# Kernel optimization log

Measured on AMD Instinct MI355X. Metric: run time of the kernel, lower is better.

Reference implementation:

```python
import jax, jax.numpy as jnp
import numpy as np
from functools import partial

EPS = 1e-6

def rmsnorm(x, w):
    rms = jnp.sqrt(jnp.mean(x * x, axis=-1, keepdims=True) + EPS)
    return x * w / rms

def causal_dwconv(x, w):
    # x: [B, T, D], w: [D, 1, k] depthwise kernel (torch Conv1d layout)
    D = x.shape[-1]
    k = w.shape[-1]
    xt = jnp.transpose(x, (0, 2, 1))  # [B, D, T]
    out = jax.lax.conv_general_dilated(
        xt, w, window_strides=(1,), padding=[(k - 1, 0)],
        dimension_numbers=("NCH", "OIH", "NCH"), feature_group_count=D)
    return jnp.transpose(out, (0, 2, 1))  # [B, T, D]

def setup_inputs() -> dict:
    key = jax.random.key(0)
    B, T, D, F, S = 2, 4096, 1024, 4096, 4096
    ks = jax.random.split(key, 20)
    s = 0.02
    return {
        "x": jax.random.normal(ks[0], (B, T, D), jnp.float32),
        "h_prev": jnp.zeros((B, D), jnp.float32),
        "norm1_w": jnp.ones((D,), jnp.float32),
        "conv3_w": jax.random.normal(ks[1], (D, 1, 3), jnp.float32) * s,
        "conv7_w": jax.random.normal(ks[2], (D, 1, 7), jnp.float32) * s,
        "conv15_w": jax.random.normal(ks[3], (D, 1, 15), jnp.float32) * s,
        "mix_w": jax.random.normal(ks[4], (D, D), jnp.float32) * s,
        "norm2_w": jnp.ones((D,), jnp.float32),
        "Wz_w": jax.random.normal(ks[5], (D, D), jnp.float32) * s,
        "Wz_b": jnp.zeros((D,), jnp.float32),
        "Wh_w": jax.random.normal(ks[6], (D, D), jnp.float32) * s,
        "Wh_b": jnp.zeros((D,), jnp.float32),
        "norm3_w": jnp.ones((D,), jnp.float32),
        "slot_keys": jax.random.normal(ks[7], (S, D), jnp.float32) * s,
        "slot_values": jax.random.normal(ks[8], (S, D), jnp.float32) * s,
        "projq_w": jax.random.normal(ks[9], (D, D), jnp.float32) * s,
        "projout_w": jax.random.normal(ks[10], (D, D), jnp.float32) * s,
        "norm4_w": jnp.ones((D,), jnp.float32),
        "gate_w": jax.random.normal(ks[11], (F, D), jnp.float32) * s,
        "up_w": jax.random.normal(ks[12], (F, D), jnp.float32) * s,
        "down_w": jax.random.normal(ks[13], (D, F), jnp.float32) * s,
    }

def resonance_forward(x, h_prev, norm1_w, conv3_w, conv7_w, conv15_w, mix_w,
                      norm2_w, Wz_w, Wz_b, Wh_w, Wh_b, norm3_w, slot_keys,
                      slot_values, projq_w, projout_w, norm4_w, gate_w, up_w, down_w):
    B, T, D = x.shape
    top_k = 2
    # 1. multi-scale causal conv block
    xn = rmsnorm(x, norm1_w)
    conv = causal_dwconv(xn, conv3_w) + causal_dwconv(xn, conv7_w) + causal_dwconv(xn, conv15_w)
    x = x + conv @ mix_w.T
    # 2. MinGRU: precompute gates, then linear recurrence via scan
    xn = rmsnorm(x, norm2_w)
    z = jax.nn.sigmoid(xn @ Wz_w.T + Wz_b)        # [B, T, D]
    h_tilde = xn @ Wh_w.T + Wh_b                  # [B, T, D]
    def step(h, zh):
        zt, ht = zh
        h = (1.0 - zt) * h + zt * ht
        return h, h
    h_last, hs = jax.lax.scan(step, h_prev,
                              (jnp.swapaxes(z, 0, 1), jnp.swapaxes(h_tilde, 0, 1)))
    x = x + jnp.swapaxes(hs, 0, 1)
    # 3. slot memory with top-k routing
    xn = rmsnorm(x, norm3_w)
    q = xn @ projq_w.T
    scores = (q @ slot_keys.T) / jnp.sqrt(jnp.asarray(D, x.dtype))  # [B, T, S]
    topk_vals, topk_ids = jax.lax.top_k(scores, top_k)              # [B, T, k]
    attn = jax.nn.softmax(topk_vals, axis=-1)
    gathered = slot_values[topk_ids]                                # [B, T, k, D]
    retrieved = jnp.einsum("btk,btkd->btd", attn, gathered)
    x = x + retrieved @ projout_w.T
    # 4. SwiGLU FFN
    xn = rmsnorm(x, norm4_w)
    ff = (jax.nn.silu(xn @ gate_w.T) * (xn @ up_w.T)) @ down_w.T
    x = x + ff
    return x, h_last

def reference(x, h_prev, norm1_w, conv3_w, conv7_w, conv15_w, mix_w, norm2_w,
              Wz_w, Wz_b, Wh_w, Wh_b, norm3_w, slot_keys, slot_values,
              projq_w, projout_w, norm4_w, gate_w, up_w, down_w):
    return resonance_forward(x, h_prev, norm1_w, conv3_w, conv7_w, conv15_w,
                             mix_w, norm2_w, Wz_w, Wz_b, Wh_w, Wh_b, norm3_w,
                             slot_keys, slot_values, projq_w, projout_w,
                             norm4_w, gate_w, up_w, down_w)
```

## Files before the change

kernel.cpp:

```cpp
#include <hip/hip_runtime.h>
#include <hip/hip_bf16.h>
#include <cstdint>

#define BB   2
#define TT   4096
#define DD   1024
#define FF   4096
#define SS   4096
#define MTOK (BB * TT)
#define NCHUNK 32
#define TCHUNK 128

typedef __bf16 bf16x8 __attribute__((ext_vector_type(8)));
typedef float  f32x4  __attribute__((ext_vector_type(4)));
typedef __attribute__((address_space(3))) char lds_char;
typedef __attribute__((address_space(1))) char g_char;

__global__ __launch_bounds__(256) void cvt_kernel(const float* __restrict__ s,
                                                  __hip_bfloat16* __restrict__ d,
                                                  int n4) {
  int i = blockIdx.x * 256 + threadIdx.x;
  if (i < n4) {
    float4 v = ((const float4*)s)[i];
    union { ushort4 u; __hip_bfloat16 h[4]; } p;
    p.h[0] = __float2bfloat16(v.x);
    p.h[1] = __float2bfloat16(v.y);
    p.h[2] = __float2bfloat16(v.z);
    p.h[3] = __float2bfloat16(v.w);
    ((ushort4*)d)[i] = p.u;
  }
}

__global__ void wcomb_kernel(const float* __restrict__ w3, const float* __restrict__ w7,
                             const float* __restrict__ w15, float* __restrict__ wc) {
  int d = blockIdx.x * 256 + threadIdx.x;
  if (d >= DD) return;
  for (int j = 0; j < 16; j++) {
    float v = 0.f;
    if (j < 15) {
      v = w15[d * 15 + (14 - j)];
      if (j < 7) v += w7[d * 7 + (6 - j)];
      if (j < 3) v += w3[d * 3 + (2 - j)];
    }
    wc[d * 16 + j] = v;
  }
}

template <int OUT_BF16>
__global__ __launch_bounds__(256) void rms_kernel(const float* __restrict__ x,
                                                  const float* __restrict__ w,
                                                  float* __restrict__ of,
                                                  __hip_bfloat16* __restrict__ ob) {
  const int row = blockIdx.x;
  const int tid = threadIdx.x;
  float4 v = ((const float4*)(x + (size_t)row * DD))[tid];
  float ss = v.x * v.x + v.y * v.y + v.z * v.z + v.w * v.w;
  for (int off = 32; off > 0; off >>= 1) ss += __shfl_down(ss, off, 64);
  __shared__ float wsum[4];
  if ((tid & 63) == 0) wsum[tid >> 6] = ss;
  __syncthreads();
  float tot = wsum[0] + wsum[1] + wsum[2] + wsum[3];
  float rinv = 1.0f / sqrtf(tot * (1.0f / DD) + 1e-6f);
  float4 wg = ((const float4*)w)[tid];
  float4 o;
  o.x = v.x * wg.x * rinv; o.y = v.y * wg.y * rinv;
  o.z = v.z * wg.z * rinv; o.w = v.w * wg.w * rinv;
  if (OUT_BF16) {
    union { ushort4 u; __hip_bfloat16 h[4]; } p;
    p.h[0] = __float2bfloat16(o.x); p.h[1] = __float2bfloat16(o.y);
    p.h[2] = __float2bfloat16(o.z); p.h[3] = __float2bfloat16(o.w);
    ((ushort4*)ob)[(size_t)row * 256 + tid] = p.u;
  } else {
    ((float4*)of)[(size_t)row * 256 + tid] = o;
  }
}

__global__ __launch_bounds__(256) void conv_kernel(const float* __restrict__ xn,
                                                   const float* __restrict__ wc,
                                                   __hip_bfloat16* __restrict__ outp) {
  __shared__ float xt[78][64];
  __shared__ float wt[64][15];
  const int b = blockIdx.z, t0 = blockIdx.x * 64, d0 = blockIdx.y * 64;
  const int tid = threadIdx.x;
  const int dl = tid & 63;
  for (int idx = tid; idx < 64 * 15; idx += 256) {
    int d = idx / 15, j = idx % 15;
    wt[d][j] = wc[(d0 + d) * 16 + j];
  }
  for (int r = tid >> 6; r < 78; r += 4) {
    int t = t0 - 14 + r;
    xt[r][dl] = (t >= 0) ? xn[((size_t)b * TT + t) * DD + d0 + dl] : 0.f;
  }
  __syncthreads();
  for (int tl = tid >> 6; tl < 64; tl += 4) {
    float acc = 0.f;
#pragma unroll
    for (int j = 0; j < 15; j++) acc += wt[dl][j] * xt[tl + 14 - j][dl];
    outp[((size_t)b * TT + t0 + tl) * DD + d0 + dl] = __float2bfloat16(acc);
  }
}

template <int EPI>
__global__ __launch_bounds__(256, 2) void gemm_bt(
    const __hip_bfloat16* __restrict__ A, const __hip_bfloat16* __restrict__ Bm,
    const int M, const int N, const int K,
    const float* __restrict__ resid, float* __restrict__ outf,
    __hip_bfloat16* __restrict__ outb,
    const float* __restrict__ bias0, const float* __restrict__ bias1,
    const __hip_bfloat16* __restrict__ mulin) {
  __shared__ __align__(16) __hip_bfloat16 As[128 * 32];
  __shared__ __align__(16) __hip_bfloat16 Bs[128 * 32];
  const int tid = threadIdx.x;
  const int lane = tid & 63;
  const int wave = tid >> 6;
  const int fm = lane & 15, fq = lane >> 4;
  const int tileN = blockIdx.x * 128;
  const int tileM = blockIdx.y * 128;
  const int wm = (wave & 1) * 64, wn = (wave >> 1) * 64;

  f32x4 acc[4][4] = {};

  const int srow = tid >> 2;
  const int scol = (tid & 3) * 8;
  const __hip_bfloat16* gA = A + (size_t)(tileM + srow) * K + scol;
  const __hip_bfloat16* gB = Bm + (size_t)(tileN + srow) * K + scol;
  lds_char* ldsA = (lds_char*)(&As[0]);
  lds_char* ldsB = (lds_char*)(&Bs[0]);
  const int wbyte = wave * 1024;

  for (int k0 = 0; k0 < K; k0 += 32) {
    __syncthreads();
    __builtin_amdgcn_global_load_lds((g_char*)(void*)(gA + k0),                  ldsA + wbyte,        16, 0, 0);
    __builtin_amdgcn_global_load_lds((g_char*)(void*)(gA + k0 + (size_t)64 * K), ldsA + wbyte + 4096, 16, 0, 0);
    __builtin_amdgcn_global_load_lds((g_char*)(void*)(gB + k0),                  ldsB + wbyte,        16, 0, 0);
    __builtin_amdgcn_global_load_lds((g_char*)(void*)(gB + k0 + (size_t)64 * K), ldsB + wbyte + 4096, 16, 0, 0);
    __syncthreads();
    bf16x8 af[4], bfr[4];
#pragma unroll
    for (int i = 0; i < 4; i++) {
      af[i]  = *(const bf16x8*)(As + (wm + i * 16 + fm) * 32 + fq * 8);
      bfr[i] = *(const bf16x8*)(Bs + (wn + i * 16 + fm) * 32 + fq * 8);
    }
#pragma unroll
    for (int i = 0; i < 4; i++)
#pragma unroll
      for (int j = 0; j < 4; j++)
        acc[i][j] = __builtin_amdgcn_mfma_f32_16x16x32_bf16(af[i], bfr[j], acc[i][j], 0, 0, 0);
  }

#pragma unroll
  for (int i = 0; i < 4; i++) {
#pragma unroll
    for (int j = 0; j < 4; j++) {
      const int c = tileN + wn + j * 16 + fm;
#pragma unroll
      for (int r = 0; r < 4; r++) {
        const int rw = tileM + wm + i * 16 + fq * 4 + r;
        const size_t idx = (size_t)rw * N + c;
        float v = acc[i][j][r];
        if constexpr (EPI == 0) {
          outf[idx] = resid[idx] + v;
        } else if constexpr (EPI == 1) {
          v += (c < DD) ? bias0[c] : bias1[c - DD];
          if (c < DD) v = 1.f / (1.f + __expf(-v));
          outf[idx] = v;
        } else if constexpr (EPI == 2) {
          outb[idx] = __float2bfloat16(v);
        } else if constexpr (EPI == 3) {
          outf[idx] = v;
        } else if constexpr (EPI == 4) {
          outb[idx] = __float2bfloat16(v / (1.f + __expf(-v)));
        } else {
          outb[idx] = __float2bfloat16(v * __bfloat162float(mulin[idx]));
        }
      }
    }
  }
}

__global__ __launch_bounds__(256) void scan_pass1(const float* __restrict__ zht,
                                                  float* __restrict__ cA,
                                                  float* __restrict__ cB) {
  const int b = blockIdx.z, c = blockIdx.y;
  const int d = blockIdx.x * 256 + threadIdx.x;
  const float* base = zht + (size_t)b * TT * 2048;
  float A = 1.f, Bc = 0.f;
  const int t0 = c * TCHUNK;
  for (int t = t0; t < t0 + TCHUNK; t++) {
    const float* rowp = base + (size_t)t * 2048;
    float z = rowp[d];
    float h = rowp[DD + d];
    float om = 1.f - z;
    A *= om;
    Bc = om * Bc + z * h;
  }
  size_t idx = ((size_t)b * NCHUNK + c) * DD + d;
  cA[idx] = A;
  cB[idx] = Bc;
}

__global__ __launch_bounds__(256) void scan_pass2(const float* __restrict__ hp,
                                                  const float* __restrict__ cA,
                                                  const float* __restrict__ cB,
                                                  float* __restrict__ hstart,
                                                  float* __restrict__ hlast) {
  const int b = blockIdx.y;
  const int d = blockIdx.x * 256 + threadIdx.x;
  float h = hp[b * DD + d];
  for (int c = 0; c < NCHUNK; c++) {
    size_t idx = ((size_t)b * NCHUNK + c) * DD + d;
    hstart[idx] = h;
    h = cA[idx] * h + cB[idx];
  }
  hlast[b * DD + d] = h;
}

__global__ __launch_bounds__(256) void scan_pass3(const float* __restrict__ zht,
                                                  const float* __restrict__ hstart,
                                                  float* __restrict__ x) {
  const int b = blockIdx.z, c = blockIdx.y;
  const int d = blockIdx.x * 256 + threadIdx.x;
  const float* base = zht + (size_t)b * TT * 2048;
  float h = hstart[((size_t)b * NCHUNK + c) * DD + d];
  const int t0 = c * TCHUNK;
  for (int t = t0; t < t0 + TCHUNK; t++) {
    const float* rowp = base + (size_t)t * 2048;
    float z = rowp[d];
    float ht = rowp[DD + d];
    h = (1.f - z) * h + z * ht;
    x[((size_t)b * TT + t) * DD + d] += h;
  }
}

__global__ __launch_bounds__(256) void topk_kernel(const float* __restrict__ scores,
                                                   const float* __restrict__ sv,
                                                   __hip_bfloat16* __restrict__ ret) {
  const int row = blockIdx.x;
  const int tid = threadIdx.x;
  const float* sr = scores + (size_t)row * SS;
  float v0 = -3.4e38f, v1 = -3.4e38f;
  int i0 = 0x7fffffff, i1 = 0x7fffffff;
  for (int j = tid; j < SS; j += 256) {
    float v = sr[j];
    if (v > v0) { v1 = v0; i1 = i0; v0 = v; i0 = j; }
    else if (v > v1) { v1 = v; i1 = j; }
  }
#define TKMERGE(w0, j0, w1, j1)                                              \
  {                                                                          \
    if (w0 > v0 || (w0 == v0 && j0 < i0)) {                                  \
      float t0v = v0; int t0i = i0; v0 = w0; i0 = j0;                        \
      if (t0v > w1 || (t0v == w1 && t0i < j1)) { v1 = t0v; i1 = t0i; }       \
      else { v1 = w1; i1 = j1; }                                             \
    } else {                                                                 \
      if (w0 > v1 || (w0 == v1 && j0 < i1)) { v1 = w0; i1 = j0; }            \
    }                                                                        \
  }
  for (int off = 32; off > 0; off >>= 1) {
    float w0 = __shfl_down(v0, off, 64), w1 = __shfl_down(v1, off, 64);
    int   j0 = __shfl_down(i0, off, 64), j1 = __shfl_down(i1, off, 64);
    TKMERGE(w0, j0, w1, j1);
  }
  __shared__ float wv0[4], wv1[4];
  __shared__ int   wi0[4], wi1[4];
  __shared__ float sattn[2];
  __shared__ int   sidx[2];
  if ((tid & 63) == 0) { int w = tid >> 6; wv0[w] = v0; wv1[w] = v1; wi0[w] = i0; wi1[w] = i1; }
  __syncthreads();
  if (tid == 0) {
    v0 = wv0[0]; i0 = wi0[0]; v1 = wv1[0]; i1 = wi1[0];
    for (int w = 1; w < 4; w++) { TKMERGE(wv0[w], wi0[w], wv1[w], wi1[w]); }
    float s0 = v0 * (1.f / 32.f), s1 = v1 * (1.f / 32.f);
    float e = __expf(s1 - s0);
    float denom = 1.f + e;
    sattn[0] = 1.f / denom;
    sattn[1] = e / denom;
    sidx[0] = i0; sidx[1] = i1;
  }
  __syncthreads();
  float a0 = sattn[0], a1 = sattn[1];
  const float4* r0 = (const float4*)(sv + (size_t)sidx[0] * DD);
  const float4* r1 = (const float4*)(sv + (size_t)sidx[1] * DD);
  float4 u = r0[tid], w4 = r1[tid];
  union { ushort4 u; __hip_bfloat16 h[4]; } p;
  p.h[0] = __float2bfloat16(a0 * u.x + a1 * w4.x);
  p.h[1] = __float2bfloat16(a0 * u.y + a1 * w4.y);
  p.h[2] = __float2bfloat16(a0 * u.z + a1 * w4.z);
  p.h[3] = __float2bfloat16(a0 * u.w + a1 * w4.w);
  ((ushort4*)(ret + (size_t)row * DD))[tid] = p.u;
#undef TKMERGE
}

extern "C" void kernel_launch(void* const* d_in, const int* in_sizes, int n_in,
                              void* d_out, int out_size, void* d_ws, size_t ws_size,
                              hipStream_t stream) {
  (void)in_sizes; (void)n_in; (void)out_size; (void)ws_size;
  const float* x_in   = (const float*)d_in[0];
  const float* h_prev = (const float*)d_in[1];
  const float* n1w    = (const float*)d_in[2];
  const float* w3     = (const float*)d_in[3];
  const float* w7     = (const float*)d_in[4];
  const float* w15    = (const float*)d_in[5];
  const float* mixw   = (const float*)d_in[6];
  const float* n2w    = (const float*)d_in[7];
  const float* wzw    = (const float*)d_in[8];
  const float* wzb    = (const float*)d_in[9];
  const float* whw    = (const float*)d_in[10];
  const float* whb    = (const float*)d_in[11];
  const float* n3w    = (const float*)d_in[12];
  const float* slotk  = (const float*)d_in[13];
  const float* slotv  = (const float*)d_in[14];
  const float* pqw    = (const float*)d_in[15];
  const float* pow_   = (const float*)d_in[16];
  const float* n4w    = (const float*)d_in[17];
  const float* gatew  = (const float*)d_in[18];
  const float* upw    = (const float*)d_in[19];
  const float* downw  = (const float*)d_in[20];
  float* out = (float*)d_out;

  char* ws = (char*)d_ws;
  size_t o = 0;
  auto alloc = [&](size_t bytes) {
    size_t r = o;
    o += (bytes + 255) & ~(size_t)255;
    return r;
  };
  __hip_bfloat16* wmix = (__hip_bfloat16*)(ws + alloc((size_t)DD * DD * 2));
  __hip_bfloat16* wzht = (__hip_bfloat16*)(ws + alloc((size_t)2 * DD * DD * 2));
  __hip_bfloat16* wpq  = (__hip_bfloat16*)(ws + alloc((size_t)DD * DD * 2));
  __hip_bfloat16* wsk  = (__hip_bfloat16*)(ws + alloc((size_t)SS * DD * 2));
  __hip_bfloat16* wpo  = (__hip_bfloat16*)(ws + alloc((size_t)DD * DD * 2));
  __hip_bfloat16* wg   = (__hip_bfloat16*)(ws + alloc((size_t)FF * DD * 2));
  __hip_bfloat16* wu   = (__hip_bfloat16*)(ws + alloc((size_t)FF * DD * 2));
  __hip_bfloat16* wd   = (__hip_bfloat16*)(ws + alloc((size_t)DD * FF * 2));
  float* wcomb = (float*)(ws + alloc((size_t)DD * 16 * 4));
  float* xws   = (float*)(ws + alloc((size_t)MTOK * DD * 4));
  __hip_bfloat16* xnb  = (__hip_bfloat16*)(ws + alloc((size_t)MTOK * DD * 2));
  __hip_bfloat16* qb   = (__hip_bfloat16*)(ws + alloc((size_t)MTOK * DD * 2));
  __hip_bfloat16* retr = (__hip_bfloat16*)(ws + alloc((size_t)MTOK * DD * 2));
  float* scanA  = (float*)(ws + alloc((size_t)BB * NCHUNK * DD * 4));
  float* scanB  = (float*)(ws + alloc((size_t)BB * NCHUNK * DD * 4));
  float* hstart = (float*)(ws + alloc((size_t)BB * NCHUNK * DD * 4));
  char* big = ws + alloc((size_t)MTOK * FF * 4);
  float* xn1f           = (float*)big;
  __hip_bfloat16* convb = (__hip_bfloat16*)(big + (size_t)MTOK * DD * 4);
  float* zht            = (float*)big;
  float* scores         = (float*)big;
  __hip_bfloat16* sg    = (__hip_bfloat16*)big;
  __hip_bfloat16* ffin  = (__hip_bfloat16*)(big + (size_t)MTOK * FF * 2);

  auto cvt = [&](const float* s, __hip_bfloat16* dp, int n) {
    cvt_kernel<<<n / 1024, 256, 0, stream>>>(s, dp, n / 4);
  };
  cvt(mixw, wmix, DD * DD);
  cvt(wzw, wzht, DD * DD);
  cvt(whw, wzht + (size_t)DD * DD, DD * DD);
  cvt(pqw, wpq, DD * DD);
  cvt(slotk, wsk, SS * DD);
  cvt(pow_, wpo, DD * DD);
  cvt(gatew, wg, FF * DD);
  cvt(upw, wu, FF * DD);
  cvt(downw, wd, DD * FF);
  wcomb_kernel<<<DD / 256, 256, 0, stream>>>(w3, w7, w15, wcomb);

  rms_kernel<0><<<MTOK, 256, 0, stream>>>(x_in, n1w, xn1f, nullptr);
  conv_kernel<<<dim3(TT / 64, DD / 64, BB), 256, 0, stream>>>(xn1f, wcomb, convb);
  gemm_bt<0><<<dim3(DD / 128, MTOK / 128), 256, 0, stream>>>(
      convb, wmix, MTOK, DD, DD, x_in, xws, nullptr, nullptr, nullptr, nullptr);

  rms_kernel<1><<<MTOK, 256, 0, stream>>>(xws, n2w, nullptr, xnb);
  gemm_bt<1><<<dim3(2048 / 128, MTOK / 128), 256, 0, stream>>>(
      xnb, wzht, MTOK, 2048, DD, nullptr, zht, nullptr, wzb, whb, nullptr);
  scan_pass1<<<dim3(DD / 256, NCHUNK, BB), 256, 0, stream>>>(zht, scanA, scanB);
  scan_pass2<<<dim3(DD / 256, BB), 256, 0, stream>>>(h_prev, scanA, scanB, hstart,
                                                     out + (size_t)MTOK * DD);
  scan_pass3<<<dim3(DD / 256, NCHUNK, BB), 256, 0, stream>>>(zht, hstart, xws);

  rms_kernel<1><<<MTOK, 256, 0, stream>>>(xws, n3w, nullptr, xnb);
  gemm_bt<2><<<dim3(DD / 128, MTOK / 128), 256, 0, stream>>>(
      xnb, wpq, MTOK, DD, DD, nullptr, nullptr, qb, nullptr, nullptr, nullptr);
  gemm_bt<3><<<dim3(SS / 128, MTOK / 128), 256, 0, stream>>>(
      qb, wsk, MTOK, SS, DD, nullptr, scores, nullptr, nullptr, nullptr, nullptr);
  topk_kernel<<<MTOK, 256, 0, stream>>>(scores, slotv, retr);
  gemm_bt<0><<<dim3(DD / 128, MTOK / 128), 256, 0, stream>>>(
      retr, wpo, MTOK, DD, DD, xws, xws, nullptr, nullptr, nullptr, nullptr);

  rms_kernel<1><<<MTOK, 256, 0, stream>>>(xws, n4w, nullptr, xnb);
  gemm_bt<4><<<dim3(FF / 128, MTOK / 128), 256, 0, stream>>>(
      xnb, wg, MTOK, FF, DD, nullptr, nullptr, sg, nullptr, nullptr, nullptr);
  gemm_bt<5><<<dim3(FF / 128, MTOK / 128), 256, 0, stream>>>(
      xnb, wu, MTOK, FF, DD, nullptr, nullptr, ffin, nullptr, nullptr, sg);
  gemm_bt<0><<<dim3(DD / 128, MTOK / 128), 256, 0, stream>>>(
      ffin, wd, MTOK, DD, FF, xws, out, nullptr, nullptr, nullptr, nullptr);
}
```

Measured before the change: 908.7 us.

## Store intermediates in bf16, fuse weight conversions, and remap GEMM tiles per XCD

Several intermediates (the norm1 output, the gate/candidate activations, and the routing scores) are now stored in bf16 instead of fp32. This roughly halves the memory traffic for the conv, scan and top-k kernels, and top-k now reads its scores with 8-wide vector loads. The nine weight conversion launches are merged into a single kernel that finds its segment through an offset table. GEMM blocks are remapped so that each XCD works on a contiguous band of M-tiles, aiming for better L2 reuse. Storing scores in bf16 risks changing top-k selection when scores are close or tied, and z/h lose precision before the scan.

```diff
diff --git a/kernel.cpp b/kernel.cpp
--- a/kernel.cpp
+++ b/kernel.cpp
@@ -16,19 +16,25 @@
 typedef __attribute__((address_space(3))) char lds_char;
 typedef __attribute__((address_space(1))) char g_char;
 
-__global__ __launch_bounds__(256) void cvt_kernel(const float* __restrict__ s,
-                                                  __hip_bfloat16* __restrict__ d,
-                                                  int n4) {
-  int i = blockIdx.x * 256 + threadIdx.x;
-  if (i < n4) {
-    float4 v = ((const float4*)s)[i];
-    union { ushort4 u; __hip_bfloat16 h[4]; } p;
-    p.h[0] = __float2bfloat16(v.x);
-    p.h[1] = __float2bfloat16(v.y);
-    p.h[2] = __float2bfloat16(v.z);
-    p.h[3] = __float2bfloat16(v.w);
-    ((ushort4*)d)[i] = p.u;
-  }
+struct CvtArgs {
+  const float* src[9];
+  __hip_bfloat16* dst[9];
+  int off4[10];
+};
+
+__global__ __launch_bounds__(256) void cvt_all_kernel(CvtArgs a) {
+  int g = blockIdx.x * 256 + threadIdx.x;
+  if (g >= a.off4[9]) return;
+  int s = 0;
+  while (g >= a.off4[s + 1]) s++;
+  int i = g - a.off4[s];
+  float4 v = ((const float4*)a.src[s])[i];
+  union { ushort4 u; __hip_bfloat16 h[4]; } p;
+  p.h[0] = __float2bfloat16(v.x);
+  p.h[1] = __float2bfloat16(v.y);
+  p.h[2] = __float2bfloat16(v.z);
+  p.h[3] = __float2bfloat16(v.w);
+  ((ushort4*)a.dst[s])[i] = p.u;
 }
 
 __global__ void wcomb_kernel(const float* __restrict__ w3, const float* __restrict__ w7,
@@ -46,10 +52,8 @@
   }
 }
 
-template <int OUT_BF16>
 __global__ __launch_bounds__(256) void rms_kernel(const float* __restrict__ x,
                                                   const float* __restrict__ w,
-                                                  float* __restrict__ of,
                                                   __hip_bfloat16* __restrict__ ob) {
   const int row = blockIdx.x;
   const int tid = threadIdx.x;
@@ -62,20 +66,15 @@
   float tot = wsum[0] + wsum[1] + wsum[2] + wsum[3];
   float rinv = 1.0f / sqrtf(tot * (1.0f / DD) + 1e-6f);
   float4 wg = ((const float4*)w)[tid];
-  float4 o;
-  o.x = v.x * wg.x * rinv; o.y = v.y * wg.y * rinv;
-  o.z = v.z * wg.z * rinv; o.w = v.w * wg.w * rinv;
-  if (OUT_BF16) {
-    union { ushort4 u; __hip_bfloat16 h[4]; } p;
-    p.h[0] = __float2bfloat16(o.x); p.h[1] = __float2bfloat16(o.y);
-    p.h[2] = __float2bfloat16(o.z); p.h[3] = __float2bfloat16(o.w);
-    ((ushort4*)ob)[(size_t)row * 256 + tid] = p.u;
-  } else {
-    ((float4*)of)[(size_t)row * 256 + tid] = o;
-  }
-}
-
-__global__ __launch_bounds__(256) void conv_kernel(const float* __restrict__ xn,
+  union { ushort4 u; __hip_bfloat16 h[4]; } p;
+  p.h[0] = __float2bfloat16(v.x * wg.x * rinv);
+  p.h[1] = __float2bfloat16(v.y * wg.y * rinv);
+  p.h[2] = __float2bfloat16(v.z * wg.z * rinv);
+  p.h[3] = __float2bfloat16(v.w * wg.w * rinv);
+  ((ushort4*)ob)[(size_t)row * 256 + tid] = p.u;
+}
+
+__global__ __launch_bounds__(256) void conv_kernel(const __hip_bfloat16* __restrict__ xn,
                                                    const float* __restrict__ wc,
                                                    __hip_bfloat16* __restrict__ outp) {
   __shared__ float xt[78][64];
@@ -89,7 +88,7 @@
   }
   for (int r = tid >> 6; r < 78; r += 4) {
     int t = t0 - 14 + r;
-    xt[r][dl] = (t >= 0) ? xn[((size_t)b * TT + t) * DD + d0 + dl] : 0.f;
+    xt[r][dl] = (t >= 0) ? __bfloat162float(xn[((size_t)b * TT + t) * DD + d0 + dl]) : 0.f;
   }
   __syncthreads();
   for (int tl = tid >> 6; tl < 64; tl += 4) {
@@ -114,8 +113,15 @@
   const int lane = tid & 63;
   const int wave = tid >> 6;
   const int fm = lane & 15, fq = lane >> 4;
-  const int tileN = blockIdx.x * 128;
-  const int tileM = blockIdx.y * 128;
+
+  const int nT = gridDim.x;
+  const int lin = blockIdx.y * nT + blockIdx.x;
+  const int xcd = lin & 7;
+  const int idx_ = lin >> 3;
+  const int mq = idx_ / nT;
+  const int tileM = (xcd * (gridDim.y >> 3) + mq) * 128;
+  const int tileN = (idx_ - mq * nT) * 128;
+
   const int wm = (wave & 1) * 64, wn = (wave >> 1) * 64;
 
   f32x4 acc[4][4] = {};
@@ -163,11 +169,9 @@
         } else if constexpr (EPI == 1) {
           v += (c < DD) ? bias0[c] : bias1[c - DD];
           if (c < DD) v = 1.f / (1.f + __expf(-v));
-          outf[idx] = v;
+          outb[idx] = __float2bfloat16(v);
         } else if constexpr (EPI == 2) {
           outb[idx] = __float2bfloat16(v);
-        } else if constexpr (EPI == 3) {
-          outf[idx] = v;
         } else if constexpr (EPI == 4) {
           outb[idx] = __float2bfloat16(v / (1.f + __expf(-v)));
         } else {
@@ -178,18 +182,18 @@
   }
 }
 
-__global__ __launch_bounds__(256) void scan_pass1(const float* __restrict__ zht,
+__global__ __launch_bounds__(256) void scan_pass1(const __hip_bfloat16* __restrict__ zht,
                                                   float* __restrict__ cA,
                                                   float* __restrict__ cB) {
   const int b = blockIdx.z, c = blockIdx.y;
   const int d = blockIdx.x * 256 + threadIdx.x;
-  const float* base = zht + (size_t)b * TT * 2048;
+  const __hip_bfloat16* base = zht + (size_t)b * TT * 2048;
   float A = 1.f, Bc = 0.f;
   const int t0 = c * TCHUNK;
   for (int t = t0; t < t0 + TCHUNK; t++) {
-    const float* rowp = base + (size_t)t * 2048;
-    float z = rowp[d];
-    float h = rowp[DD + d];
+    const __hip_bfloat16* rowp = base + (size_t)t * 2048;
+    float z = __bfloat162float(rowp[d]);
+    float h = __bfloat162float(rowp[DD + d]);
     float om = 1.f - z;
     A *= om;
     Bc = om * Bc + z * h;
@@ -215,35 +219,42 @@
   hlast[b * DD + d] = h;
 }
 
-__global__ __launch_bounds__(256) void scan_pass3(const float* __restrict__ zht,
+__global__ __launch_bounds__(256) void scan_pass3(const __hip_bfloat16* __restrict__ zht,
                                                   const float* __restrict__ hstart,
                                                   float* __restrict__ x) {
   const int b = blockIdx.z, c = blockIdx.y;
   const int d = blockIdx.x * 256 + threadIdx.x;
-  const float* base = zht + (size_t)b * TT * 2048;
+  const __hip_bfloat16* base = zht + (size_t)b * TT * 2048;
   float h = hstart[((size_t)b * NCHUNK + c) * DD + d];
   const int t0 = c * TCHUNK;
   for (int t = t0; t < t0 + TCHUNK; t++) {
-    const float* rowp = base + (size_t)t * 2048;
-    float z = rowp[d];
-    float ht = rowp[DD + d];
+    const __hip_bfloat16* rowp = base + (size_t)t * 2048;
+    float z = __bfloat162float(rowp[d]);
+    float ht = __bfloat162float(rowp[DD + d]);
     h = (1.f - z) * h + z * ht;
     x[((size_t)b * TT + t) * DD + d] += h;
   }
 }
 
-__global__ __launch_bounds__(256) void topk_kernel(const float* __restrict__ scores,
+__global__ __launch_bounds__(256) void topk_kernel(const __hip_bfloat16* __restrict__ scores,
                                                    const float* __restrict__ sv,
                                                    __hip_bfloat16* __restrict__ ret) {
   const int row = blockIdx.x;
   const int tid = threadIdx.x;
-  const float* sr = scores + (size_t)row * SS;
+  const __hip_bfloat16* sr = scores + (size_t)row * SS;
   float v0 = -3.4e38f, v1 = -3.4e38f;
   int i0 = 0x7fffffff, i1 = 0x7fffffff;
-  for (int j = tid; j < SS; j += 256) {
-    float v = sr[j];
-    if (v > v0) { v1 = v0; i1 = i0; v0 = v; i0 = j; }
-    else if (v > v1) { v1 = v; i1 = j; }
+#pragma unroll
+  for (int it = 0; it < 2; it++) {
+    int j0 = (it * 256 + tid) * 8;
+    bf16x8 v8 = *(const bf16x8*)(sr + j0);
+#pragma unroll
+    for (int k = 0; k < 8; k++) {
+      float v = (float)v8[k];
+      int j = j0 + k;
+      if (v > v0) { v1 = v0; i1 = i0; v0 = v; i0 = j; }
+      else if (v > v1) { v1 = v; i1 = j; }
+    }
   }
 #define TKMERGE(w0, j0, w1, j1)                                              \
   {                                                                          \
@@ -341,50 +352,49 @@
   float* scanB  = (float*)(ws + alloc((size_t)BB * NCHUNK * DD * 4));
   float* hstart = (float*)(ws + alloc((size_t)BB * NCHUNK * DD * 4));
   char* big = ws + alloc((size_t)MTOK * FF * 4);
-  float* xn1f           = (float*)big;
-  __hip_bfloat16* convb = (__hip_bfloat16*)(big + (size_t)MTOK * DD * 4);
-  float* zht            = (float*)big;
-  float* scores         = (float*)big;
+  __hip_bfloat16* xn1b  = (__hip_bfloat16*)big;
+  __hip_bfloat16* convb = (__hip_bfloat16*)(big + (size_t)MTOK * DD * 2);
+  __hip_bfloat16* zhtb  = (__hip_bfloat16*)big;
+  __hip_bfloat16* scoresb = (__hip_bfloat16*)big;
   __hip_bfloat16* sg    = (__hip_bfloat16*)big;
   __hip_bfloat16* ffin  = (__hip_bfloat16*)(big + (size_t)MTOK * FF * 2);
 
-  auto cvt = [&](const float* s, __hip_bfloat16* dp, int n) {
-    cvt_kernel<<<n / 1024, 256, 0, stream>>>(s, dp, n / 4);
-  };
-  cvt(mixw, wmix, DD * DD);
-  cvt(wzw, wzht, DD * DD);
-  cvt(whw, wzht + (size_t)DD * DD, DD * DD);
-  cvt(pqw, wpq, DD * DD);
-  cvt(slotk, wsk, SS * DD);
-  cvt(pow_, wpo, DD * DD);
-  cvt(gatew, wg, FF * DD);
-  cvt(upw, wu, FF * DD);
-  cvt(downw, wd, DD * FF);
+  {
+    CvtArgs a;
+    const float* srcs[9] = {mixw, wzw, whw, pqw, slotk, pow_, gatew, upw, downw};
+    __hip_bfloat16* dsts[9] = {wmix, wzht, wzht + (size_t)DD * DD, wpq, wsk, wpo, wg, wu, wd};
+    int n4s[9] = {DD * DD / 4, DD * DD / 4, DD * DD / 4, DD * DD / 4, SS * DD / 4,
+                  DD * DD / 4, FF * DD / 4, FF * DD / 4, DD * FF / 4};
+    int acc_ = 0;
+    for (int i = 0; i < 9; i++) { a.src[i] = srcs[i]; a.dst[i] = dsts[i]; a.off4[i] = acc_; acc_ += n4s[i]; }
+    a.off4[9] = acc_;
+    cvt_all_kernel<<<(acc_ + 255) / 256, 256, 0, stream>>>(a);
+  }
   wcomb_kernel<<<DD / 256, 256, 0, stream>>>(w3, w7, w15, wcomb);
 
-  rms_kernel<0><<<MTOK, 256, 0, stream>>>(x_in, n1w, xn1f, nullptr);
-  conv_kernel<<<dim3(TT / 64, DD / 64, BB), 256, 0, stream>>>(xn1f, wcomb, convb);
+  rms_kernel<<<MTOK, 256, 0, stream>>>(x_in, n1w, xn1b);
+  conv_kernel<<<dim3(TT / 64, DD / 64, BB), 256, 0, stream>>>(xn1b, wcomb, convb);
   gemm_bt<0><<<dim3(DD / 128, MTOK / 128), 256, 0, stream>>>(
       convb, wmix, MTOK, DD, DD, x_in, xws, nullptr, nullptr, nullptr, nullptr);
 
-  rms_kernel<1><<<MTOK, 256, 0, stream>>>(xws, n2w, nullptr, xnb);
+  rms_kernel<<<MTOK, 256, 0, stream>>>(xws, n2w, xnb);
   gemm_bt<1><<<dim3(2048 / 128, MTOK / 128), 256, 0, stream>>>(
-      xnb, wzht, MTOK, 2048, DD, nullptr, zht, nullptr, wzb, whb, nullptr);
-  scan_pass1<<<dim3(DD / 256, NCHUNK, BB), 256, 0, stream>>>(zht, scanA, scanB);
+      xnb, wzht, MTOK, 2048, DD, nullptr, nullptr, zhtb, wzb, whb, nullptr);
+  scan_pass1<<<dim3(DD / 256, NCHUNK, BB), 256, 0, stream>>>(zhtb, scanA, scanB);
   scan_pass2<<<dim3(DD / 256, BB), 256, 0, stream>>>(h_prev, scanA, scanB, hstart,
                                                      out + (size_t)MTOK * DD);
-  scan_pass3<<<dim3(DD / 256, NCHUNK, BB), 256, 0, stream>>>(zht, hstart, xws);
-
-  rms_kernel<1><<<MTOK, 256, 0, stream>>>(xws, n3w, nullptr, xnb);
+  scan_pass3<<<dim3(DD / 256, NCHUNK, BB), 256, 0, stream>>>(zhtb, hstart, xws);
+
+  rms_kernel<<<MTOK, 256, 0, stream>>>(xws, n3w, xnb);
   gemm_bt<2><<<dim3(DD / 128, MTOK / 128), 256, 0, stream>>>(
       xnb, wpq, MTOK, DD, DD, nullptr, nullptr, qb, nullptr, nullptr, nullptr);
-  gemm_bt<3><<<dim3(SS / 128, MTOK / 128), 256, 0, stream>>>(
-      qb, wsk, MTOK, SS, DD, nullptr, scores, nullptr, nullptr, nullptr, nullptr);
-  topk_kernel<<<MTOK, 256, 0, stream>>>(scores, slotv, retr);
+  gemm_bt<2><<<dim3(SS / 128, MTOK / 128), 256, 0, stream>>>(
+      qb, wsk, MTOK, SS, DD, nullptr, nullptr, scoresb, nullptr, nullptr, nullptr);
+  topk_kernel<<<MTOK, 256, 0, stream>>>(scoresb, slotv, retr);
   gemm_bt<0><<<dim3(DD / 128, MTOK / 128), 256, 0, stream>>>(
       retr, wpo, MTOK, DD, DD, xws, xws, nullptr, nullptr, nullptr, nullptr);
 
-  rms_kernel<1><<<MTOK, 256, 0, stream>>>(xws, n4w, nullptr, xnb);
+  rms_kernel<<<MTOK, 256, 0, stream>>>(xws, n4w, xnb);
   gemm_bt<4><<<dim3(FF / 128, MTOK / 128), 256, 0, stream>>>(
       xnb, wg, MTOK, FF, DD, nullptr, nullptr, sg, nullptr, nullptr, nullptr);
   gemm_bt<5><<<dim3(FF / 128, MTOK / 128), 256, 0, stream>>>(
```

Result: faster. 799.7 us (-12.0%).
